# Kernel optimization log

Hardware: AMD Instinct MI355X
Metric: run time of the kernel (lower is better)

The kernel has to match this reference:

```python
import jax, jax.numpy as jnp
import numpy as np

B, C_IN, C_OUT, N, L = 4, 128, 256, 4096, 4
D = C_OUT // 4
EPS_BN = 1e-5


def setup_inputs() -> dict:
    key = jax.random.key(0)
    ks = jax.random.split(key, 16)
    s_in = 1.0 / np.sqrt(C_IN)
    s_out = 1.0 / np.sqrt(C_OUT)
    return {
        "features": jax.random.normal(ks[0], (B, C_IN, N), dtype=jnp.float32),
        # LBR: conv1x1 -> BN -> ReLU -> conv1x1 -> BN -> ReLU
        "lbr_w1": jax.random.uniform(ks[1], (C_OUT, C_IN), jnp.float32, -s_in, s_in),
        "lbr_g1": jnp.ones((C_OUT,), jnp.float32),
        "lbr_b1": jnp.zeros((C_OUT,), jnp.float32),
        "lbr_w2": jax.random.uniform(ks[2], (C_OUT, C_OUT), jnp.float32, -s_out, s_out),
        "lbr_g2": jnp.ones((C_OUT,), jnp.float32),
        "lbr_b2": jnp.zeros((C_OUT,), jnp.float32),
        # per-layer OffsetAttention params (stacked on leading L axis)
        # q_conv and k_conv share the same weight (q_conv.weight = k_conv.weight)
        "attn_qk_w": jax.random.uniform(ks[3], (L, D, C_OUT), jnp.float32, -s_out, s_out),
        "attn_v_w": jax.random.uniform(ks[4], (L, C_OUT, C_OUT), jnp.float32, -s_out, s_out),
        "attn_v_b": jax.random.uniform(ks[5], (L, C_OUT), jnp.float32, -s_out, s_out),
        "attn_t_w": jax.random.uniform(ks[6], (L, C_OUT, C_OUT), jnp.float32, -s_out, s_out),
        "attn_t_b": jax.random.uniform(ks[7], (L, C_OUT), jnp.float32, -s_out, s_out),
        "attn_bn_g": jnp.ones((L, C_OUT), jnp.float32),
        "attn_bn_b": jnp.zeros((L, C_OUT), jnp.float32),
    }


def batchnorm1d(x, gamma, beta):
    # x: [B, C, N]; training-mode BN: batch stats over (B, N), biased variance
    mean = jnp.mean(x, axis=(0, 2), keepdims=True)
    var = jnp.mean(jnp.square(x - mean), axis=(0, 2), keepdims=True)
    xn = (x - mean) * jax.lax.rsqrt(var + EPS_BN)
    return xn * gamma[None, :, None] + beta[None, :, None]


def offset_attention(x, qk_w, v_w, v_b, t_w, t_b, bn_g, bn_b):
    # x: [B, C, N]
    K = jnp.einsum("dc,bcn->bdn", qk_w, x)            # [B, D, N]
    # Q = same conv, permuted to [B, N, D]; attention_map = Q @ K -> [B, N, N]
    attn = jnp.einsum("bdn,bdm->bnm", K, K)
    attn = jax.nn.softmax(attn, axis=-1)
    # extra L1 renorm over dim=1 (column-wise)
    attn = attn / (1e-9 + jnp.sum(attn, axis=1, keepdims=True))
    V = jnp.einsum("dc,bcn->bdn", v_w, x) + v_b[None, :, None]  # [B, C, N]
    new_feat = jnp.einsum("bcn,bnm->bcm", V, attn)    # [B, C, N]
    off = x - new_feat
    t = jnp.einsum("dc,bcn->bdn", t_w, off) + t_b[None, :, None]
    return jax.nn.relu(batchnorm1d(t, bn_g, bn_b))


def reference(features, lbr_w1, lbr_g1, lbr_b1, lbr_w2, lbr_g2, lbr_b2,
              attn_qk_w, attn_v_w, attn_v_b, attn_t_w, attn_t_b,
              attn_bn_g, attn_bn_b):
    # LBR stem
    h = jnp.einsum("dc,bcn->bdn", lbr_w1, features)
    h = jax.nn.relu(batchnorm1d(h, lbr_g1, lbr_b1))
    h = jnp.einsum("dc,bcn->bdn", lbr_w2, h)
    h = jax.nn.relu(batchnorm1d(h, lbr_g2, lbr_b2))
    # stacked offset attention; output concatenates attention outputs only
    outs = []
    cur = h
    for i in range(L):
        cur = offset_attention(cur, attn_qk_w[i], attn_v_w[i], attn_v_b[i],
                               attn_t_w[i], attn_t_b[i], attn_bn_g[i], attn_bn_b[i])
        outs.append(cur)
    return jnp.concatenate(outs, axis=1)  # [B, C_OUT*L, N]
```

## Files before the change

kernel.cpp:

```cpp
#include <hip/hip_runtime.h>
#include <hip/hip_bf16.h>
#include <math.h>

#define NPTS 4096
#define CO   256
#define CI   128
#define BB   4
#define DQ   64
#define LL   4
#define PST  136

typedef __attribute__((ext_vector_type(8))) short bf16x8;
typedef __attribute__((ext_vector_type(4))) float f32x4;

#define MFMA16(a,b,c) __builtin_amdgcn_mfma_f32_16x16x32_bf16((a),(b),(c),0,0,0)

__device__ __forceinline__ short fb(float x) {
  __hip_bfloat16 h = __float2bfloat16(x);
  return __builtin_bit_cast(short, h);
}
__device__ __forceinline__ float bf(short s) {
  unsigned u = ((unsigned)(unsigned short)s) << 16;
  return __builtin_bit_cast(float, u);
}

__global__ __launch_bounds__(256) void cvt5_k(
    const float* __restrict__ s1, short* __restrict__ d1, int n1,
    const float* __restrict__ s2, short* __restrict__ d2, int n2,
    const float* __restrict__ s3, short* __restrict__ d3, int n3,
    const float* __restrict__ s4, short* __restrict__ d4, int n4,
    const float* __restrict__ s5, short* __restrict__ d5, int n5)
{
  int i = blockIdx.x * 256 + threadIdx.x;
  const float* S; short* D;
  if      (i < n1)                       { S = s1; D = d1; }
  else if ((i -= n1) < n2)               { S = s2; D = d2; }
  else if ((i -= n2) < n3)               { S = s3; D = d3; }
  else if ((i -= n3) < n4)               { S = s4; D = d4; }
  else if ((i -= n4) < n5)               { S = s5; D = d5; }
  else return;
  const float4 a = ((const float4*)S)[i * 2];
  const float4 b = ((const float4*)S)[i * 2 + 1];
  bf16x8 r;
  r[0] = fb(a.x); r[1] = fb(a.y); r[2] = fb(a.z); r[3] = fb(a.w);
  r[4] = fb(b.x); r[5] = fb(b.y); r[6] = fb(b.z); r[7] = fb(b.w);
  ((bf16x8*)D)[i] = r;
}

__global__ __launch_bounds__(256) void tcvt_k(
    const float* __restrict__ X, long xbs, int C, short* __restrict__ XT)
{
  const int n0 = blockIdx.x * 64, c0 = blockIdx.y * 64, b = blockIdx.z;
  const int t = threadIdx.x, tl = t & 63, tg = t >> 6;
  __shared__ float xs[64][65];
#pragma unroll
  for (int r = 0; r < 16; ++r) {
    const int cc = tg * 16 + r;
    xs[cc][tl] = X[(long)b * xbs + (long)(c0 + cc) * NPTS + n0 + tl];
  }
  __syncthreads();
#pragma unroll
  for (int r = 0; r < 16; ++r) {
    const int nn = tg * 16 + r;
    XT[((long)b * NPTS + n0 + nn) * C + c0 + tl] = fb(xs[tl][nn]);
  }
}

template<int OMODE, bool BIAS>
__global__ __launch_bounds__(256) void conv_a(
    const short* __restrict__ XT, int C,
    const short* __restrict__ Wb, const float* __restrict__ bias,
    short* __restrict__ Yv, long ybs,
    float* __restrict__ ps1, float* __restrict__ ps2)
{
  const int n0 = blockIdx.x * 64, d0 = blockIdx.y * 64, b = blockIdx.z;
  const int tid = threadIdx.x, w = tid >> 6, l = tid & 63, lg = l >> 4, lr = l & 15;
  const short* xb = XT + (long)b * NPTS * C;
  f32x4 acc[4];
#pragma unroll
  for (int i = 0; i < 4; ++i) acc[i] = (f32x4){0.f, 0.f, 0.f, 0.f};
  const int dr = d0 + w * 16 + lr;
  for (int kc = 0; kc < C; kc += 32) {
    const bf16x8 af = *(const bf16x8*)&Wb[(long)dr * C + kc + lg * 8];
#pragma unroll
    for (int ni = 0; ni < 4; ++ni) {
      const bf16x8 bx = *(const bf16x8*)&xb[(long)(n0 + ni * 16 + lr) * C + kc + lg * 8];
      acc[ni] = MFMA16(af, bx, acc[ni]);
    }
  }
  float bv[4] = {0.f, 0.f, 0.f, 0.f};
  if (BIAS) {
    const float4 b4 = *(const float4*)&bias[d0 + w * 16 + lg * 4];
    bv[0] = b4.x; bv[1] = b4.y; bv[2] = b4.z; bv[3] = b4.w;
  }
  const int db = d0 + w * 16 + lg * 4;
  float s1[4], s2[4];
#pragma unroll
  for (int j = 0; j < 4; ++j) { s1[j] = 0.f; s2[j] = 0.f; }
#pragma unroll
  for (int ni = 0; ni < 4; ++ni) {
    const int n = n0 + ni * 16 + lr;
#pragma unroll
    for (int j = 0; j < 4; ++j) {
      const short ob = fb(acc[ni][j] + bv[j]);
      if constexpr (OMODE == 1) {
        Yv[(long)b * ybs + ((long)(n >> 7) * CO + db + j) * 128 + (n & 127)] = ob;
      } else {
        Yv[(long)b * ybs + (long)(db + j) * NPTS + n] = ob;
        const float o = bf(ob);
        s1[j] += o; s2[j] += o * o;
      }
    }
  }
  if constexpr (OMODE == 2) {
#pragma unroll
    for (int j = 0; j < 4; ++j) {
#pragma unroll
      for (int off = 1; off < 16; off <<= 1) {
        s1[j] += __shfl_xor(s1[j], off);
        s2[j] += __shfl_xor(s2[j], off);
      }
    }
    if (lr == 0) {
      const int slot = b * 64 + blockIdx.x;
#pragma unroll
      for (int j = 0; j < 4; ++j) {
        ps1[(long)(db + j) * 256 + slot] = s1[j];
        ps2[(long)(db + j) * 256 + slot] = s2[j];
      }
    }
  }
}

__global__ __launch_bounds__(256) void conv_b(
    const short* __restrict__ XT, const short* __restrict__ Wb,
    short* __restrict__ KTo, float* __restrict__ nrm2)
{
  const int n0 = blockIdx.x * 64, b = blockIdx.y;
  const int tid = threadIdx.x, w = tid >> 6, l = tid & 63, lg = l >> 4, lr = l & 15;
  const short* xb = XT + (long)b * NPTS * CO;
  f32x4 acc[4];
#pragma unroll
  for (int i = 0; i < 4; ++i) acc[i] = (f32x4){0.f, 0.f, 0.f, 0.f};
  const long nr = n0 + w * 16 + lr;
  for (int kc = 0; kc < CO; kc += 32) {
    const bf16x8 af = *(const bf16x8*)&xb[nr * CO + kc + lg * 8];
#pragma unroll
    for (int di = 0; di < 4; ++di) {
      const bf16x8 wf = *(const bf16x8*)&Wb[(long)(di * 16 + lr) * CO + kc + lg * 8];
      acc[di] = MFMA16(af, wf, acc[di]);
    }
  }
  short* Ko = KTo + (long)b * NPTS * DQ;
  const int nb = n0 + w * 16 + lg * 4;
  float nv[4];
#pragma unroll
  for (int j = 0; j < 4; ++j) {
    nv[j] = 0.f;
#pragma unroll
    for (int di = 0; di < 4; ++di) {
      Ko[(long)(nb + j) * DQ + di * 16 + lr] = fb(acc[di][j]);
      nv[j] = fmaf(acc[di][j], acc[di][j], nv[j]);
    }
  }
#pragma unroll
  for (int j = 0; j < 4; ++j) {
#pragma unroll
    for (int off = 1; off < 16; off <<= 1) nv[j] += __shfl_xor(nv[j], off);
  }
  if (lr == 0) {
#pragma unroll
    for (int j = 0; j < 4; ++j) nrm2[(long)b * NPTS + nb + j] = nv[j];
  }
}

__global__ __launch_bounds__(256) void bound_k(
    const float* __restrict__ nrm2, float* __restrict__ rmax)
{
  const int b = blockIdx.x, t = threadIdx.x;
  __shared__ float red[4];
  float mx = 0.f;
  for (int n = t; n < NPTS; n += 256) mx = fmaxf(mx, nrm2[(long)b * NPTS + n]);
#pragma unroll
  for (int o = 32; o > 0; o >>= 1) mx = fmaxf(mx, __shfl_down(mx, o));
  if ((t & 63) == 0) red[t >> 6] = mx;
  __syncthreads();
  const float mv = fmaxf(fmaxf(red[0], red[1]), fmaxf(red[2], red[3]));
  for (int n = t; n < NPTS; n += 256)
    rmax[(long)b * NPTS + n] = sqrtf(nrm2[(long)b * NPTS + n] * mv);
}

__global__ __launch_bounds__(64) void bnfin_k(
    const float* __restrict__ ps1, const float* __restrict__ ps2,
    float* __restrict__ mean, float* __restrict__ rstd)
{
  const int c = blockIdx.x, t = threadIdx.x;
  float s = 0.f, s2 = 0.f;
#pragma unroll
  for (int i = 0; i < 4; ++i) {
    s  += ps1[(long)c * 256 + t + i * 64];
    s2 += ps2[(long)c * 256 + t + i * 64];
  }
#pragma unroll
  for (int o = 32; o > 0; o >>= 1) { s += __shfl_down(s, o); s2 += __shfl_down(s2, o); }
  if (t == 0) {
    const float m = s / (float)(BB * NPTS);
    const float v = s2 / (float)(BB * NPTS) - m * m;
    mean[c] = m;
    rstd[c] = rsqrtf(v + 1e-5f);
  }
}

template<bool WF32, bool WBF>
__global__ __launch_bounds__(256) void bnrelu_t(
    const short* __restrict__ X, long xbs,
    const float* __restrict__ mean, const float* __restrict__ rstd,
    const float* __restrict__ g, const float* __restrict__ be,
    float* __restrict__ Yf, long ybs, short* __restrict__ XT)
{
  const int n0 = blockIdx.x * 64, c0 = blockIdx.y * 64, b = blockIdx.z;
  const int t = threadIdx.x, tl = t & 63, tg = t >> 6;
  __shared__ float xs[64][65];
#pragma unroll
  for (int r = 0; r < 16; ++r) {
    const int cc = tg * 16 + r, c = c0 + cc;
    float v = bf(X[(long)b * xbs + (long)c * NPTS + n0 + tl]);
    v = fmaxf((v - mean[c]) * rstd[c] * g[c] + be[c], 0.f);
    if (WF32) Yf[(long)b * ybs + (long)c * NPTS + n0 + tl] = v;
    xs[cc][tl] = v;
  }
  __syncthreads();
  if (WBF) {
#pragma unroll
    for (int r = 0; r < 16; ++r) {
      const int nn = tg * 16 + r;
      XT[((long)b * NPTS + n0 + nn) * CO + c0 + tl] = fb(xs[tl][nn]);
    }
  }
}

__global__ __launch_bounds__(256) void rowsum_mfma(
    const short* __restrict__ KT, const float* __restrict__ rmax,
    float* __restrict__ psum)
{
  const int bid = blockIdx.x;
  const int b = (bid >> 1) & 3;
  const int idx = (bid >> 3) * 2 + (bid & 1);
  const int n0 = (idx & 63) * 64;
  const int chunk = idx >> 6;
  const int tid = threadIdx.x, w = tid >> 6, l = tid & 63, lg = l >> 4, lr = l & 15;
  const short* Kb = KT + (long)b * NPTS * DQ;
  const int nr = n0 + w * 16 + lr;
  const bf16x8 a0 = *(const bf16x8*)&Kb[(long)nr * DQ + lg * 8];
  const bf16x8 a1 = *(const bf16x8*)&Kb[(long)nr * DQ + 32 + lg * 8];
  const float4 M4 = *(const float4*)&rmax[(long)b * NPTS + n0 + w * 16 + lg * 4];

  float sm[4][4];
#pragma unroll
  for (int p = 0; p < 4; ++p)
#pragma unroll
    for (int j = 0; j < 4; ++j) sm[p][j] = 0.f;

  const int mc = chunk * (NPTS / 4);
  for (int m0 = mc; m0 < mc + NPTS / 4; m0 += 64) {
#pragma unroll
    for (int p = 0; p < 4; ++p) {
      const bf16x8 b0 = *(const bf16x8*)&Kb[(long)(m0 + p * 16 + lr) * DQ + lg * 8];
      const bf16x8 b1 = *(const bf16x8*)&Kb[(long)(m0 + p * 16 + lr) * DQ + 32 + lg * 8];
      f32x4 s = {0.f, 0.f, 0.f, 0.f};
      s = MFMA16(a0, b0, s);
      s = MFMA16(a1, b1, s);
      sm[p][0] += __expf(s[0] - M4.x);
      sm[p][1] += __expf(s[1] - M4.y);
      sm[p][2] += __expf(s[2] - M4.z);
      sm[p][3] += __expf(s[3] - M4.w);
    }
  }
  float sf[4];
#pragma unroll
  for (int j = 0; j < 4; ++j)
    sf[j] = (sm[0][j] + sm[1][j]) + (sm[2][j] + sm[3][j]);
#pragma unroll
  for (int off = 1; off < 16; off <<= 1)
#pragma unroll
    for (int j = 0; j < 4; ++j) sf[j] += __shfl_xor(sf[j], off);

  if (lr == 0) {
    const long base = ((long)chunk * BB + b) * NPTS + n0 + w * 16 + lg * 4;
#pragma unroll
    for (int j = 0; j < 4; ++j) psum[base + j] = sf[j];
  }
}

__global__ __launch_bounds__(256) void combine_sum(
    const float* __restrict__ psum, float* __restrict__ rinv)
{
  const long i = (long)blockIdx.x * 256 + threadIdx.x;
  const long st = (long)BB * NPTS;
  rinv[i] = 1.f / ((psum[i] + psum[st + i]) + (psum[2 * st + i] + psum[3 * st + i]));
}

__global__ __launch_bounds__(512) void pass2_mfma(
    const short* __restrict__ KT, const short* __restrict__ Vblk,
    const float* __restrict__ rmax, const float* __restrict__ rinv,
    short* __restrict__ XO)
{
  const int bid = blockIdx.x;
  const int b  = (bid >> 1) & 3;
  const int m0 = ((bid >> 3) * 2 + (bid & 1)) * 64;
  const int tid = threadIdx.x;
  const int w = tid >> 6, l = tid & 63, lg = l >> 4, lr = l & 15;

  const short* Kb = KT + (long)b * NPTS * DQ;
  const short* Vb = Vblk + (long)b * CO * NPTS;
  const float* rmb = rmax + (long)b * NPTS;
  const float* rib = rinv + (long)b * NPTS;

  __shared__ short Ps[2][64][PST];
  __shared__ float cspart[8][64];
  __shared__ float csum[64];

  bf16x8 bK[4][2];
#pragma unroll
  for (int ms = 0; ms < 4; ++ms) {
    bK[ms][0] = *(const bf16x8*)&Kb[(long)(m0 + ms * 16 + lr) * DQ + lg * 8];
    bK[ms][1] = *(const bf16x8*)&Kb[(long)(m0 + ms * 16 + lr) * DQ + 32 + lg * 8];
  }

  f32x4 acc[4][2];
#pragma unroll
  for (int i = 0; i < 4; ++i) {
    acc[i][0] = (f32x4){0.f, 0.f, 0.f, 0.f};
    acc[i][1] = (f32x4){0.f, 0.f, 0.f, 0.f};
  }
  float cs[4] = {0.f, 0.f, 0.f, 0.f};
  const int c0 = w * 32;
  const int nb = w * 16;

  bf16x8 a0 = *(const bf16x8*)&Kb[(long)(nb + lr) * DQ + lg * 8];
  bf16x8 a1 = *(const bf16x8*)&Kb[(long)(nb + lr) * DQ + 32 + lg * 8];
  float4 rm4 = *(const float4*)&rmb[nb + lg * 4];
  float4 ri4 = *(const float4*)&rib[nb + lg * 4];

  int buf = 0;
  for (int n0 = 0; n0 < NPTS; n0 += 128) {
    const short* vt = Vb + (long)(n0 >> 7) * CO * 128;
    bf16x8 vf[4][2];
#pragma unroll
    for (int kc = 0; kc < 4; ++kc) {
      vf[kc][0] = *(const bf16x8*)&vt[(long)(c0 + lr) * 128 + kc * 32 + lg * 8];
      vf[kc][1] = *(const bf16x8*)&vt[(long)(c0 + 16 + lr) * 128 + kc * 32 + lg * 8];
    }
    f32x4 s[4];
#pragma unroll
    for (int ms = 0; ms < 4; ++ms) {
      s[ms] = (f32x4){0.f, 0.f, 0.f, 0.f};
      s[ms] = MFMA16(a0, bK[ms][0], s[ms]);
      s[ms] = MFMA16(a1, bK[ms][1], s[ms]);
    }
#pragma unroll
    for (int ms = 0; ms < 4; ++ms) {
      const float p0 = __expf(s[ms][0] - rm4.x) * ri4.x;
      const float p1 = __expf(s[ms][1] - rm4.y) * ri4.y;
      const float p2 = __expf(s[ms][2] - rm4.z) * ri4.z;
      const float p3 = __expf(s[ms][3] - rm4.w) * ri4.w;
      cs[ms] += p0 + p1 + p2 + p3;
      const unsigned u0 = ((unsigned)(unsigned short)fb(p1) << 16) | (unsigned short)fb(p0);
      const unsigned u1 = ((unsigned)(unsigned short)fb(p3) << 16) | (unsigned short)fb(p2);
      *(uint2*)&Ps[buf][ms * 16 + lr][nb + lg * 4] = make_uint2(u0, u1);
    }
    asm volatile("s_waitcnt lgkmcnt(0)" ::: "memory");
    __builtin_amdgcn_s_barrier();
    if (n0 + 128 < NPTS) {
      a0  = *(const bf16x8*)&Kb[(long)(n0 + 128 + nb + lr) * DQ + lg * 8];
      a1  = *(const bf16x8*)&Kb[(long)(n0 + 128 + nb + lr) * DQ + 32 + lg * 8];
      rm4 = *(const float4*)&rmb[n0 + 128 + nb + lg * 4];
      ri4 = *(const float4*)&rib[n0 + 128 + nb + lg * 4];
    }
#pragma unroll
    for (int kc = 0; kc < 4; ++kc) {
      bf16x8 pa[4];
#pragma unroll
      for (int ms = 0; ms < 4; ++ms)
        pa[ms] = *(const bf16x8*)&Ps[buf][ms * 16 + lr][kc * 32 + lg * 8];
#pragma unroll
      for (int ms = 0; ms < 4; ++ms) {
        acc[ms][0] = MFMA16(pa[ms], vf[kc][0], acc[ms][0]);
        acc[ms][1] = MFMA16(pa[ms], vf[kc][1], acc[ms][1]);
      }
    }
    buf ^= 1;
  }

  __syncthreads();
#pragma unroll
  for (int ms = 0; ms < 4; ++ms) {
    float csv = cs[ms];
    csv += __shfl_xor(csv, 16); csv += __shfl_xor(csv, 32);
    if (lg == 0) cspart[w][ms * 16 + lr] = csv;
  }
  __syncthreads();
  if (tid < 64) {
    float s = 0.f;
#pragma unroll
    for (int ww = 0; ww < 8; ++ww) s += cspart[ww][tid];
    csum[tid] = s;
  }
  __syncthreads();

  short* XOb = XO + (long)b * NPTS * CO;
#pragma unroll
  for (int ms = 0; ms < 4; ++ms) {
#pragma unroll
    for (int j = 0; j < 4; ++j) {
      const int m = m0 + ms * 16 + lg * 4 + j;
      const float inv = 1.f / (1e-9f + csum[ms * 16 + lg * 4 + j]);
      const long i0 = (long)m * CO + c0 + lr;
      const long i1 = (long)m * CO + c0 + 16 + lr;
      XOb[i0] = fb(bf(XOb[i0]) - acc[ms][0][j] * inv);
      XOb[i1] = fb(bf(XOb[i1]) - acc[ms][1][j] * inv);
    }
  }
}

extern "C" void kernel_launch(void* const* d_in, const int* in_sizes, int n_in,
                              void* d_out, int out_size, void* d_ws, size_t ws_size,
                              hipStream_t stream)
{
  const float* feat = (const float*)d_in[0];
  const float* w1   = (const float*)d_in[1];
  const float* g1   = (const float*)d_in[2];
  const float* b1   = (const float*)d_in[3];
  const float* w2   = (const float*)d_in[4];
  const float* g2   = (const float*)d_in[5];
  const float* b2   = (const float*)d_in[6];
  const float* qkw  = (const float*)d_in[7];
  const float* vw   = (const float*)d_in[8];
  const float* vb   = (const float*)d_in[9];
  const float* tw   = (const float*)d_in[10];
  const float* tb   = (const float*)d_in[11];
  const float* bng  = (const float*)d_in[12];
  const float* bnb  = (const float*)d_in[13];

  float* out = (float*)d_out;

  short* xt    = (short*)d_ws;
  short* KTb   = xt + (long)BB * NPTS * CO;
  short* Vblk  = KTb + (long)BB * NPTS * DQ;
  short* wb1   = Vblk + (long)BB * CO * NPTS;
  short* wb2   = wb1 + (long)CO * CI;
  short* wqk   = wb2 + (long)CO * CO;
  short* wv    = wqk + (long)LL * DQ * CO;
  short* wt    = wv + (long)LL * CO * CO;
  float* psumb = (float*)(wt + (long)LL * CO * CO);
  float* nrm2b = psumb + (long)4 * BB * NPTS;
  float* rmaxb = nrm2b + (long)BB * NPTS;
  float* rinvb = rmaxb + (long)BB * NPTS;
  float* ps1   = rinvb + (long)BB * NPTS;
  float* ps2   = ps1 + (long)CO * 256;
  float* meanb = ps2 + (long)CO * 256;
  float* rstdb = meanb + CO;

  const long OBS = (long)LL * CO * NPTS;
  const long TBS = (long)CO * NPTS;
  short* pre = Vblk;

  const dim3 blk(256);

  {
    const int n1 = CO * CI / 8, n2 = CO * CO / 8, n3 = LL * DQ * CO / 8,
              n4 = LL * CO * CO / 8, n5 = LL * CO * CO / 8;
    const int tot = n1 + n2 + n3 + n4 + n5;
    cvt5_k<<<dim3((tot + 255) / 256), blk, 0, stream>>>(
        w1, wb1, n1, w2, wb2, n2, qkw, wqk, n3, vw, wv, n4, tw, wt, n5);
  }

  tcvt_k<<<dim3(64, 2, BB), blk, 0, stream>>>(feat, (long)CI * NPTS, CI, xt);
  conv_a<2, false><<<dim3(64, 4, BB), blk, 0, stream>>>(
      xt, CI, wb1, nullptr, pre, TBS, ps1, ps2);
  bnfin_k<<<dim3(CO), dim3(64), 0, stream>>>(ps1, ps2, meanb, rstdb);
  bnrelu_t<false, true><<<dim3(64, 4, BB), blk, 0, stream>>>(
      pre, TBS, meanb, rstdb, g1, b1, nullptr, 0, xt);
  conv_a<2, false><<<dim3(64, 4, BB), blk, 0, stream>>>(
      xt, CO, wb2, nullptr, pre, TBS, ps1, ps2);
  bnfin_k<<<dim3(CO), dim3(64), 0, stream>>>(ps1, ps2, meanb, rstdb);
  bnrelu_t<false, true><<<dim3(64, 4, BB), blk, 0, stream>>>(
      pre, TBS, meanb, rstdb, g2, b2, nullptr, 0, xt);

  for (int lyr = 0; lyr < LL; ++lyr) {
    float* nft = out + (long)lyr * CO * NPTS;
    conv_b<<<dim3(64, BB), blk, 0, stream>>>(xt, wqk + (long)lyr * DQ * CO, KTb, nrm2b);
    bound_k<<<dim3(BB), blk, 0, stream>>>(nrm2b, rmaxb);
    conv_a<1, true><<<dim3(64, 4, BB), blk, 0, stream>>>(
        xt, CO, wv + (long)lyr * CO * CO, vb + (long)lyr * CO, Vblk, TBS, nullptr, nullptr);
    rowsum_mfma<<<dim3(1024), blk, 0, stream>>>(KTb, rmaxb, psumb);
    combine_sum<<<dim3(BB * NPTS / 256), blk, 0, stream>>>(psumb, rinvb);
    pass2_mfma<<<dim3(256), dim3(512), 0, stream>>>(KTb, Vblk, rmaxb, rinvb, xt);
    conv_a<2, true><<<dim3(64, 4, BB), blk, 0, stream>>>(
        xt, CO, wt + (long)lyr * CO * CO, tb + (long)lyr * CO, pre, TBS, ps1, ps2);
    bnfin_k<<<dim3(CO), dim3(64), 0, stream>>>(ps1, ps2, meanb, rstdb);
    if (lyr < LL - 1) {
      bnrelu_t<true, true><<<dim3(64, 4, BB), blk, 0, stream>>>(
          pre, TBS, meanb, rstdb, bng + (long)lyr * CO, bnb + (long)lyr * CO, nft, OBS, xt);
    } else {
      bnrelu_t<true, false><<<dim3(64, 4, BB), blk, 0, stream>>>(
          pre, TBS, meanb, rstdb, bng + (long)lyr * CO, bnb + (long)lyr * CO, nft, OBS, nullptr);
    }
  }
}
```

Before: 917.5 us.

## Fuse K and V projections into one launch and prefetch V tiles in pass2

The K projection and V projection convolutions now run as one kernel whose block index picks which job each block does. This removes one launch per layer and lets the two run at the same time. In pass2, the loop is unrolled by two with separate register sets for V fragments, so the next V tile is loaded from global memory while the current tile's MFMAs run. This raises register pressure and may lower occupancy. The V conv is rewritten inline, replacing the conv_a<1,true> path.

```diff
diff --git a/kernel.cpp b/kernel.cpp
--- a/kernel.cpp
+++ b/kernel.cpp
@@ -132,45 +132,77 @@
   }
 }
 
-__global__ __launch_bounds__(256) void conv_b(
-    const short* __restrict__ XT, const short* __restrict__ Wb,
-    short* __restrict__ KTo, float* __restrict__ nrm2)
-{
-  const int n0 = blockIdx.x * 64, b = blockIdx.y;
+__global__ __launch_bounds__(256) void conv_kv(
+    const short* __restrict__ XT,
+    const short* __restrict__ Wk, short* __restrict__ KTo, float* __restrict__ nrm2,
+    const short* __restrict__ Wv, const float* __restrict__ vbias,
+    short* __restrict__ Vblk)
+{
   const int tid = threadIdx.x, w = tid >> 6, l = tid & 63, lg = l >> 4, lr = l & 15;
-  const short* xb = XT + (long)b * NPTS * CO;
-  f32x4 acc[4];
-#pragma unroll
-  for (int i = 0; i < 4; ++i) acc[i] = (f32x4){0.f, 0.f, 0.f, 0.f};
-  const long nr = n0 + w * 16 + lr;
-  for (int kc = 0; kc < CO; kc += 32) {
-    const bf16x8 af = *(const bf16x8*)&xb[nr * CO + kc + lg * 8];
-#pragma unroll
-    for (int di = 0; di < 4; ++di) {
-      const bf16x8 wf = *(const bf16x8*)&Wb[(long)(di * 16 + lr) * CO + kc + lg * 8];
-      acc[di] = MFMA16(af, wf, acc[di]);
-    }
-  }
-  short* Ko = KTo + (long)b * NPTS * DQ;
-  const int nb = n0 + w * 16 + lg * 4;
-  float nv[4];
-#pragma unroll
-  for (int j = 0; j < 4; ++j) {
-    nv[j] = 0.f;
-#pragma unroll
-    for (int di = 0; di < 4; ++di) {
-      Ko[(long)(nb + j) * DQ + di * 16 + lr] = fb(acc[di][j]);
-      nv[j] = fmaf(acc[di][j], acc[di][j], nv[j]);
-    }
-  }
-#pragma unroll
-  for (int j = 0; j < 4; ++j) {
-#pragma unroll
-    for (int off = 1; off < 16; off <<= 1) nv[j] += __shfl_xor(nv[j], off);
-  }
-  if (lr == 0) {
-#pragma unroll
-    for (int j = 0; j < 4; ++j) nrm2[(long)b * NPTS + nb + j] = nv[j];
+  const int bid = blockIdx.x;
+  if (bid < BB * 64) {
+    const int n0 = (bid & 63) * 64, b = bid >> 6;
+    const short* xb = XT + (long)b * NPTS * CO;
+    f32x4 acc[4];
+#pragma unroll
+    for (int i = 0; i < 4; ++i) acc[i] = (f32x4){0.f, 0.f, 0.f, 0.f};
+    const long nr = n0 + w * 16 + lr;
+    for (int kc = 0; kc < CO; kc += 32) {
+      const bf16x8 af = *(const bf16x8*)&xb[nr * CO + kc + lg * 8];
+#pragma unroll
+      for (int di = 0; di < 4; ++di) {
+        const bf16x8 wf = *(const bf16x8*)&Wk[(long)(di * 16 + lr) * CO + kc + lg * 8];
+        acc[di] = MFMA16(af, wf, acc[di]);
+      }
+    }
+    short* Ko = KTo + (long)b * NPTS * DQ;
+    const int nb = n0 + w * 16 + lg * 4;
+    float nv[4];
+#pragma unroll
+    for (int j = 0; j < 4; ++j) {
+      nv[j] = 0.f;
+#pragma unroll
+      for (int di = 0; di < 4; ++di) {
+        Ko[(long)(nb + j) * DQ + di * 16 + lr] = fb(acc[di][j]);
+        nv[j] = fmaf(acc[di][j], acc[di][j], nv[j]);
+      }
+    }
+#pragma unroll
+    for (int j = 0; j < 4; ++j) {
+#pragma unroll
+      for (int off = 1; off < 16; off <<= 1) nv[j] += __shfl_xor(nv[j], off);
+    }
+    if (lr == 0) {
+#pragma unroll
+      for (int j = 0; j < 4; ++j) nrm2[(long)b * NPTS + nb + j] = nv[j];
+    }
+  } else {
+    const int id = bid - BB * 64;
+    const int n0 = (id & 63) * 64, d0 = ((id >> 6) & 3) * 64, b = id >> 8;
+    const short* xb = XT + (long)b * NPTS * CO;
+    f32x4 acc[4];
+#pragma unroll
+    for (int i = 0; i < 4; ++i) acc[i] = (f32x4){0.f, 0.f, 0.f, 0.f};
+    const int dr = d0 + w * 16 + lr;
+    for (int kc = 0; kc < CO; kc += 32) {
+      const bf16x8 af = *(const bf16x8*)&Wv[(long)dr * CO + kc + lg * 8];
+#pragma unroll
+      for (int ni = 0; ni < 4; ++ni) {
+        const bf16x8 bx = *(const bf16x8*)&xb[(long)(n0 + ni * 16 + lr) * CO + kc + lg * 8];
+        acc[ni] = MFMA16(af, bx, acc[ni]);
+      }
+    }
+    const float4 b4 = *(const float4*)&vbias[d0 + w * 16 + lg * 4];
+    const float bv[4] = {b4.x, b4.y, b4.z, b4.w};
+    const int db = d0 + w * 16 + lg * 4;
+#pragma unroll
+    for (int ni = 0; ni < 4; ++ni) {
+      const int n = n0 + ni * 16 + lr;
+#pragma unroll
+      for (int j = 0; j < 4; ++j)
+        Vblk[(long)b * CO * NPTS + ((long)(n >> 7) * CO + db + j) * 128 + (n & 127)] =
+            fb(acc[ni][j] + bv[j]);
+    }
   }
 }
 
@@ -337,20 +369,25 @@
   const int c0 = w * 32;
   const int nb = w * 16;
 
-  bf16x8 a0 = *(const bf16x8*)&Kb[(long)(nb + lr) * DQ + lg * 8];
-  bf16x8 a1 = *(const bf16x8*)&Kb[(long)(nb + lr) * DQ + 32 + lg * 8];
-  float4 rm4 = *(const float4*)&rmb[nb + lg * 4];
-  float4 ri4 = *(const float4*)&rib[nb + lg * 4];
-
-  int buf = 0;
-  for (int n0 = 0; n0 < NPTS; n0 += 128) {
-    const short* vt = Vb + (long)(n0 >> 7) * CO * 128;
-    bf16x8 vf[4][2];
+  bf16x8 a0, a1;
+  float4 rm4, ri4;
+  bf16x8 vfA[4][2], vfB[4][2];
+
+  auto vload = [&](bf16x8 (&vf)[4][2], int n0v) {
+    const short* vt = Vb + (long)(n0v >> 7) * CO * 128;
 #pragma unroll
     for (int kc = 0; kc < 4; ++kc) {
       vf[kc][0] = *(const bf16x8*)&vt[(long)(c0 + lr) * 128 + kc * 32 + lg * 8];
       vf[kc][1] = *(const bf16x8*)&vt[(long)(c0 + 16 + lr) * 128 + kc * 32 + lg * 8];
     }
+  };
+  auto kload = [&](int n0k) {
+    a0  = *(const bf16x8*)&Kb[(long)(n0k + nb + lr) * DQ + lg * 8];
+    a1  = *(const bf16x8*)&Kb[(long)(n0k + nb + lr) * DQ + 32 + lg * 8];
+    rm4 = *(const float4*)&rmb[n0k + nb + lg * 4];
+    ri4 = *(const float4*)&rib[n0k + nb + lg * 4];
+  };
+  auto phaseA = [&](short (*PsB)[PST]) {
     f32x4 s[4];
 #pragma unroll
     for (int ms = 0; ms < 4; ++ms) {
@@ -367,29 +404,41 @@
       cs[ms] += p0 + p1 + p2 + p3;
       const unsigned u0 = ((unsigned)(unsigned short)fb(p1) << 16) | (unsigned short)fb(p0);
       const unsigned u1 = ((unsigned)(unsigned short)fb(p3) << 16) | (unsigned short)fb(p2);
-      *(uint2*)&Ps[buf][ms * 16 + lr][nb + lg * 4] = make_uint2(u0, u1);
-    }
-    asm volatile("s_waitcnt lgkmcnt(0)" ::: "memory");
-    __builtin_amdgcn_s_barrier();
-    if (n0 + 128 < NPTS) {
-      a0  = *(const bf16x8*)&Kb[(long)(n0 + 128 + nb + lr) * DQ + lg * 8];
-      a1  = *(const bf16x8*)&Kb[(long)(n0 + 128 + nb + lr) * DQ + 32 + lg * 8];
-      rm4 = *(const float4*)&rmb[n0 + 128 + nb + lg * 4];
-      ri4 = *(const float4*)&rib[n0 + 128 + nb + lg * 4];
-    }
+      *(uint2*)&PsB[ms * 16 + lr][nb + lg * 4] = make_uint2(u0, u1);
+    }
+  };
+  auto phaseB = [&](short (*PsB)[PST], const bf16x8 (&vf)[4][2]) {
 #pragma unroll
     for (int kc = 0; kc < 4; ++kc) {
       bf16x8 pa[4];
 #pragma unroll
       for (int ms = 0; ms < 4; ++ms)
-        pa[ms] = *(const bf16x8*)&Ps[buf][ms * 16 + lr][kc * 32 + lg * 8];
+        pa[ms] = *(const bf16x8*)&PsB[ms * 16 + lr][kc * 32 + lg * 8];
 #pragma unroll
       for (int ms = 0; ms < 4; ++ms) {
         acc[ms][0] = MFMA16(pa[ms], vf[kc][0], acc[ms][0]);
         acc[ms][1] = MFMA16(pa[ms], vf[kc][1], acc[ms][1]);
       }
     }
-    buf ^= 1;
+  };
+
+  vload(vfA, 0);
+  kload(0);
+
+  for (int it = 0; it < NPTS / 128; it += 2) {
+    const int n0 = it * 128;
+    vload(vfB, n0 + 128);
+    phaseA(Ps[0]);
+    asm volatile("s_waitcnt lgkmcnt(0)" ::: "memory");
+    __builtin_amdgcn_s_barrier();
+    kload(n0 + 128);
+    phaseB(Ps[0], vfA);
+    if (it + 2 < NPTS / 128) vload(vfA, n0 + 256);
+    phaseA(Ps[1]);
+    asm volatile("s_waitcnt lgkmcnt(0)" ::: "memory");
+    __builtin_amdgcn_s_barrier();
+    if (it + 2 < NPTS / 128) kload(n0 + 256);
+    phaseB(Ps[1], vfB);
   }
 
   __syncthreads();
@@ -489,10 +538,10 @@
 
   for (int lyr = 0; lyr < LL; ++lyr) {
     float* nft = out + (long)lyr * CO * NPTS;
-    conv_b<<<dim3(64, BB), blk, 0, stream>>>(xt, wqk + (long)lyr * DQ * CO, KTb, nrm2b);
+    conv_kv<<<dim3(BB * 64 + BB * 4 * 64), blk, 0, stream>>>(
+        xt, wqk + (long)lyr * DQ * CO, KTb, nrm2b,
+        wv + (long)lyr * CO * CO, vb + (long)lyr * CO, Vblk);
     bound_k<<<dim3(BB), blk, 0, stream>>>(nrm2b, rmaxb);
-    conv_a<1, true><<<dim3(64, 4, BB), blk, 0, stream>>>(
-        xt, CO, wv + (long)lyr * CO * CO, vb + (long)lyr * CO, Vblk, TBS, nullptr, nullptr);
     rowsum_mfma<<<dim3(1024), blk, 0, stream>>>(KTb, rmaxb, psumb);
     combine_sum<<<dim3(BB * NPTS / 256), blk, 0, stream>>>(psumb, rinvb);
     pass2_mfma<<<dim3(256), dim3(512), 0, stream>>>(KTb, Vblk, rmaxb, rinvb, xt);
```

Measured after the change: 939.3 us. 2.4% more time.
